# Kernel optimization log

Hardware: AMD Instinct MI355X
Metric: run time of the kernel (lower is better)

The kernel has to match this reference:

```python
import jax, jax.numpy as jnp
import numpy as np

NG, NT, E = 2500, 20000, 640000
SRC_DIM, DST_DIM, HID, OUT, NCLS = 128, 500, 128, 128, 16


def setup_inputs() -> dict:
    key = jax.random.key(0)
    ks = jax.random.split(key, 11)
    d = {
        "gene_feats": jax.random.normal(ks[0], (NG, SRC_DIM), jnp.float32),
        "train_feats": jax.random.normal(ks[1], (NT, DST_DIM), jnp.float32),
        "edge_src": jax.random.randint(ks[2], (E,), 0, NG),
        "edge_dst": jax.random.randint(ks[3], (E,), 0, NT),
        # conv1: SAGEConv((src_dim, dst_dim) -> hidden)
        "W1_neigh": jax.random.normal(ks[4], (SRC_DIM, HID), jnp.float32) / np.sqrt(SRC_DIM),
        "W1_self": jax.random.normal(ks[5], (DST_DIM, HID), jnp.float32) / np.sqrt(DST_DIM),
        "b1": jnp.zeros((HID,), jnp.float32),
        # conv2: SAGEConv(hidden -> out); src input is the raw gene features
        "W2_neigh": jax.random.normal(ks[6], (HID, OUT), jnp.float32) / np.sqrt(HID),
        "W2_self": jax.random.normal(ks[7], (HID, OUT), jnp.float32) / np.sqrt(HID),
        "b2": jnp.zeros((OUT,), jnp.float32),
        # classifier MLP
        "Wc1": jax.random.normal(ks[8], (OUT, OUT), jnp.float32) / np.sqrt(OUT),
        "bc1": jnp.zeros((OUT,), jnp.float32),
        "Wc2": jax.random.normal(ks[9], (OUT, NCLS), jnp.float32) / np.sqrt(OUT),
        "bc2": jnp.zeros((NCLS,), jnp.float32),
    }
    return d


def _segment_mean(msgs, dst, num_segments):
    # mean over in-edges; isolated dst nodes get 0 (DGL convention)
    sums = jax.ops.segment_sum(msgs, dst, num_segments=num_segments)
    cnt = jax.ops.segment_sum(jnp.ones((msgs.shape[0],), msgs.dtype), dst,
                              num_segments=num_segments)
    return sums / jnp.maximum(cnt, 1.0)[:, None]


def reference(gene_feats, train_feats, edge_src, edge_dst,
              W1_neigh, W1_self, b1, W2_neigh, W2_self, b2,
              Wc1, bc1, Wc2, bc2):
    # mean-aggregate gene (src) features onto train (dst) nodes
    agg = _segment_mean(gene_feats[edge_src], edge_dst, NT)  # [NT, SRC_DIM]
    # conv1: fc_self(h_dst) + fc_neigh(mean_neigh) + bias, then ReLU
    h1 = jax.nn.relu(train_feats @ W1_self + agg @ W1_neigh + b1)  # [NT, HID]
    # conv2 reuses raw gene features as src -> same mean aggregation
    h2 = jax.nn.relu(h1 @ W2_self + agg @ W2_neigh + b2)  # [NT, OUT]
    # classifier: Linear -> ReLU -> Linear
    return jax.nn.relu(h2 @ Wc1 + bc1) @ Wc2 + bc2  # [NT, NCLS]
```

## Files before the change

### kernel.cpp

```cpp
#include <hip/hip_runtime.h>


#define NG 2500
#define NT 20000
#define NE 640000
#define NCLS 16
#define CAP 96
#define NTILE 1250

typedef unsigned short u16;
typedef unsigned int u32;

typedef float f32x4 __attribute__((ext_vector_type(4)));
typedef __bf16 bf16x8 __attribute__((ext_vector_type(8)));

__device__ __forceinline__ float b2f(u16 u) { return __uint_as_float(((u32)u) << 16); }
__device__ __forceinline__ float blo(u32 p) { return __uint_as_float(p << 16); }
__device__ __forceinline__ float bhi(u32 p) { return __uint_as_float(p & 0xffff0000u); }
__device__ __forceinline__ u16 f2b(float f) {
    u32 u = __float_as_uint(f);
    return (u16)((u + 0x7fffu + ((u >> 16) & 1u)) >> 16);
}

#define B1N 81920
#define B2N 32768
#define B3N 16384
#define B4N 2048
#define NEB 2500
#define CVB NTILE
#define GNB 625
#define PKB 520

__global__ __launch_bounds__(256) void k_prep(
    const int* __restrict__ esrc, const int* __restrict__ edst,
    int* __restrict__ cnt, u16* __restrict__ csr,
    const float* __restrict__ train, const float* __restrict__ gene,
    u16* __restrict__ AF, u32* __restrict__ GH32,
    const float* __restrict__ W1n, const float* __restrict__ W1s,
    const float* __restrict__ W2n, const float* __restrict__ W2s,
    const float* __restrict__ Wc1, const float* __restrict__ Wc2,
    u16* __restrict__ B1h, u16* __restrict__ B1l,
    u16* __restrict__ B2h, u16* __restrict__ B2l,
    u16* __restrict__ B3h, u16* __restrict__ B3l,
    u16* __restrict__ B4h, u16* __restrict__ B4l) {
    int blk = blockIdx.x, t = threadIdx.x;
    if (blk < NEB) {
        int e = blk * 256 + t;
        if (e < NE) {
            unsigned d = (unsigned)edst[e];
            if (d < NT) {
                int slot = atomicAdd(&cnt[d], 1);
                if (slot < CAP) csr[(size_t)d * CAP + slot] = (u16)esrc[e];
            }
        }
        return;
    }
    if (blk < NEB + CVB) {
        __shared__ __align__(16) u16 L[16 * 520];
        u32* L32 = (u32*)L;
        int tile = blk - NEB;
        for (int i = t; i < 160; i += 256) {
            int r = i / 10, c = i - r * 10;
            L32[r * 260 + 250 + c] = 0;
        }
        for (int i = t; i < 2000; i += 256) {
            int r = i / 125, c4 = i - r * 125;
            float4 v = *(const float4*)(train + (size_t)(tile * 16 + r) * 500 + c4 * 4);
            int base = r * 260 + c4 * 2;
            L32[base] = (u32)f2b(v.x) | ((u32)f2b(v.y) << 16);
            L32[base + 1] = (u32)f2b(v.z) | ((u32)f2b(v.w) << 16);
        }
        __syncthreads();
#pragma unroll
        for (int it = 0; it < 4; ++it) {
            int slot = t + it * 256;
            int kk = slot >> 6, lane = slot & 63;
            int m = lane & 15, q = lane >> 4;
            uint4 v = *(const uint4*)(L + m * 520 + kk * 32 + q * 8);
            *(uint4*)(AF + (((size_t)tile * 16 + kk) * 64 + lane) * 8) = v;
        }
        return;
    }
    if (blk < NEB + CVB + GNB) {
        int idx = (blk - NEB - CVB) * 256 + t;
        float2 v = ((const float2*)gene)[idx];
        GH32[idx] = (u32)f2b(v.x) | ((u32)f2b(v.y) << 16);
        return;
    }
    int idx = (blk - NEB - CVB - GNB) * 256 + t;
    float v = 0.f;
    u16 *ph = 0, *pl = 0;
    int off = 0;
    if (idx < B1N) {
        int j = idx & 7, l = (idx >> 3) & 63, rest = idx >> 9;
        int g = rest & 7, kk = rest >> 3;
        int k = kk * 32 + ((l >> 4) << 3) + j, n = (g << 4) + (l & 15);
        if (k < 500) v = W1s[k * 128 + n];
        else if (k >= 512) v = W1n[(k - 512) * 128 + n];
        ph = B1h; pl = B1l; off = idx;
    } else if (idx < B1N + B2N) {
        int e = idx - B1N;
        int j = e & 7, l = (e >> 3) & 63, rest = e >> 9;
        int g = rest & 7, kk = rest >> 3;
        int k = kk * 32 + ((l >> 4) << 3) + j, n = (g << 4) + (l & 15);
        v = (k < 128) ? W2s[k * 128 + n] : W2n[(k - 128) * 128 + n];
        ph = B2h; pl = B2l; off = e;
    } else if (idx < B1N + B2N + B3N) {
        int e = idx - (B1N + B2N);
        int j = e & 7, l = (e >> 3) & 63, rest = e >> 9;
        int g = rest & 7, kk = rest >> 3;
        int k = kk * 32 + ((l >> 4) << 3) + j, n = (g << 4) + (l & 15);
        v = Wc1[k * 128 + n];
        ph = B3h; pl = B3l; off = e;
    } else if (idx < B1N + B2N + B3N + B4N) {
        int e = idx - (B1N + B2N + B3N);
        int j = e & 7, l = (e >> 3) & 63, kk = e >> 9;
        int k = kk * 32 + ((l >> 4) << 3) + j, n = l & 15;
        v = Wc2[k * 16 + n];
        ph = B4h; pl = B4l; off = e;
    }
    if (ph) {
        u16 hi = f2b(v);
        u16 lo = f2b(v - b2f(hi));
        ph[off] = hi;
        pl[off] = lo;
    }
}

__global__ __launch_bounds__(512) void k_mega(
    const int* __restrict__ cnt, const u16* __restrict__ csr,
    const u16* __restrict__ GH, const u16* __restrict__ AF,
    const u16* __restrict__ B1h, const u16* __restrict__ B1l,
    const u16* __restrict__ B2h, const u16* __restrict__ B2l,
    const u16* __restrict__ B3h, const u16* __restrict__ B3l,
    const u16* __restrict__ B4h, const u16* __restrict__ B4l,
    const float* __restrict__ b1, const float* __restrict__ b2,
    const float* __restrict__ bc1, const float* __restrict__ bc2,
    float* __restrict__ out) {
    __shared__ __align__(16) u16 SAGh[32 * 136], SAGl[32 * 136];
    __shared__ __align__(16) u16 S1h[32 * 136], S1l[32 * 136];
    __shared__ __align__(16) u16 S2h[32 * 136], S2l[32 * 136];
    int t = threadIdx.x;
    int row0 = blockIdx.x * 32;

    {
        int r = t >> 4, cg = t & 15;
        int d = row0 + r;
        int ctrue = cnt[d];
        int c = ctrue > CAP ? CAP : ctrue;
        const u16* crow = csr + (size_t)d * CAP;
        float a[8];
#pragma unroll
        for (int p = 0; p < 8; ++p) a[p] = 0.f;
        int j = 0;
        for (; j + 1 < c; j += 2) {
            int s0 = crow[j], s1 = crow[j + 1];
            uint4 p0 = *(const uint4*)(GH + (size_t)s0 * 128 + cg * 8);
            uint4 p1 = *(const uint4*)(GH + (size_t)s1 * 128 + cg * 8);
            a[0] += blo(p0.x); a[1] += bhi(p0.x);
            a[2] += blo(p0.y); a[3] += bhi(p0.y);
            a[4] += blo(p0.z); a[5] += bhi(p0.z);
            a[6] += blo(p0.w); a[7] += bhi(p0.w);
            a[0] += blo(p1.x); a[1] += bhi(p1.x);
            a[2] += blo(p1.y); a[3] += bhi(p1.y);
            a[4] += blo(p1.z); a[5] += bhi(p1.z);
            a[6] += blo(p1.w); a[7] += bhi(p1.w);
        }
        if (j < c) {
            int s = crow[j];
            uint4 p0 = *(const uint4*)(GH + (size_t)s * 128 + cg * 8);
            a[0] += blo(p0.x); a[1] += bhi(p0.x);
            a[2] += blo(p0.y); a[3] += bhi(p0.y);
            a[4] += blo(p0.z); a[5] += bhi(p0.z);
            a[6] += blo(p0.w); a[7] += bhi(p0.w);
        }
        float inv = (ctrue > 0) ? 1.f / (float)ctrue : 0.f;
        int base = (r * 136 + cg * 8) >> 1;
        u32* SH = (u32*)SAGh;
        u32* SL = (u32*)SAGl;
#pragma unroll
        for (int p = 0; p < 4; ++p) {
            float x = a[2 * p] * inv, y = a[2 * p + 1] * inv;
            u16 hx = f2b(x), hy = f2b(y);
            SH[base + p] = (u32)hx | ((u32)hy << 16);
            SL[base + p] = (u32)f2b(x - b2f(hx)) | ((u32)f2b(y - b2f(hy)) << 16);
        }
    }
    __syncthreads();

    int lane = t & 63, g = t >> 6;
    int m = lane & 15, q = lane >> 4, n16 = lane & 15;
    size_t tile0 = (size_t)blockIdx.x * 2;

    const u16* aB0 = AF + ((tile0 * 16) * 64 + lane) * 8;
    const u16* aB1 = AF + (((tile0 + 1) * 16) * 64 + lane) * 8;
    int hr0 = m * 136 + q * 8;
    int hr1 = (16 + m) * 136 + q * 8;
    int cr0 = q * 4, cr1 = 16 + q * 4;
    const f32x4 z4 = {0.f, 0.f, 0.f, 0.f};
    f32x4 acc0 = z4, acc1 = z4;

#pragma unroll 4
    for (int kk = 0; kk < 16; ++kk) {
        bf16x8 a0 = *(const bf16x8*)(aB0 + kk * 512);
        bf16x8 a1 = *(const bf16x8*)(aB1 + kk * 512);
        size_t bo = ((size_t)(kk * 8 + g) * 64 + lane) * 8;
        bf16x8 bh = *(const bf16x8*)(B1h + bo);
        bf16x8 bl = *(const bf16x8*)(B1l + bo);
        acc0 = __builtin_amdgcn_mfma_f32_16x16x32_bf16(a0, bh, acc0, 0, 0, 0);
        acc0 = __builtin_amdgcn_mfma_f32_16x16x32_bf16(a0, bl, acc0, 0, 0, 0);
        acc1 = __builtin_amdgcn_mfma_f32_16x16x32_bf16(a1, bh, acc1, 0, 0, 0);
        acc1 = __builtin_amdgcn_mfma_f32_16x16x32_bf16(a1, bl, acc1, 0, 0, 0);
    }
#pragma unroll
    for (int kk = 16; kk < 20; ++kk) {
        int o = (kk - 16) * 32;
        bf16x8 ah0 = *(const bf16x8*)(SAGh + hr0 + o);
        bf16x8 al0 = *(const bf16x8*)(SAGl + hr0 + o);
        bf16x8 ah1 = *(const bf16x8*)(SAGh + hr1 + o);
        bf16x8 al1 = *(const bf16x8*)(SAGl + hr1 + o);
        size_t bo = ((size_t)(kk * 8 + g) * 64 + lane) * 8;
        bf16x8 bh = *(const bf16x8*)(B1h + bo);
        bf16x8 bl = *(const bf16x8*)(B1l + bo);
        acc0 = __builtin_amdgcn_mfma_f32_16x16x32_bf16(ah0, bh, acc0, 0, 0, 0);
        acc0 = __builtin_amdgcn_mfma_f32_16x16x32_bf16(ah0, bl, acc0, 0, 0, 0);
        acc0 = __builtin_amdgcn_mfma_f32_16x16x32_bf16(al0, bh, acc0, 0, 0, 0);
        acc1 = __builtin_amdgcn_mfma_f32_16x16x32_bf16(ah1, bh, acc1, 0, 0, 0);
        acc1 = __builtin_amdgcn_mfma_f32_16x16x32_bf16(ah1, bl, acc1, 0, 0, 0);
        acc1 = __builtin_amdgcn_mfma_f32_16x16x32_bf16(al1, bh, acc1, 0, 0, 0);
    }
    {
        int n = g * 16 + n16;
        float bias = b1[n];
#pragma unroll
        for (int rg = 0; rg < 4; ++rg) {
            float v0 = acc0[rg] + bias; v0 = v0 > 0.f ? v0 : 0.f;
            float v1 = acc1[rg] + bias; v1 = v1 > 0.f ? v1 : 0.f;
            u16 h0 = f2b(v0), h1v = f2b(v1);
            S1h[(cr0 + rg) * 136 + n] = h0; S1l[(cr0 + rg) * 136 + n] = f2b(v0 - b2f(h0));
            S1h[(cr1 + rg) * 136 + n] = h1v; S1l[(cr1 + rg) * 136 + n] = f2b(v1 - b2f(h1v));
        }
    }
    __syncthreads();

    acc0 = z4; acc1 = z4;
#pragma unroll
    for (int kk = 0; kk < 8; ++kk) {
        const u16* Ph = (kk < 4) ? S1h : SAGh;
        const u16* Pl = (kk < 4) ? S1l : SAGl;
        int o = (kk & 3) * 32;
        bf16x8 ah0 = *(const bf16x8*)(Ph + hr0 + o);
        bf16x8 al0 = *(const bf16x8*)(Pl + hr0 + o);
        bf16x8 ah1 = *(const bf16x8*)(Ph + hr1 + o);
        bf16x8 al1 = *(const bf16x8*)(Pl + hr1 + o);
        size_t bo = ((size_t)(kk * 8 + g) * 64 + lane) * 8;
        bf16x8 bh = *(const bf16x8*)(B2h + bo);
        bf16x8 bl = *(const bf16x8*)(B2l + bo);
        acc0 = __builtin_amdgcn_mfma_f32_16x16x32_bf16(ah0, bh, acc0, 0, 0, 0);
        acc0 = __builtin_amdgcn_mfma_f32_16x16x32_bf16(ah0, bl, acc0, 0, 0, 0);
        acc0 = __builtin_amdgcn_mfma_f32_16x16x32_bf16(al0, bh, acc0, 0, 0, 0);
        acc1 = __builtin_amdgcn_mfma_f32_16x16x32_bf16(ah1, bh, acc1, 0, 0, 0);
        acc1 = __builtin_amdgcn_mfma_f32_16x16x32_bf16(ah1, bl, acc1, 0, 0, 0);
        acc1 = __builtin_amdgcn_mfma_f32_16x16x32_bf16(al1, bh, acc1, 0, 0, 0);
    }
    {
        int n = g * 16 + n16;
        float bias = b2[n];
#pragma unroll
        for (int rg = 0; rg < 4; ++rg) {
            float v0 = acc0[rg] + bias; v0 = v0 > 0.f ? v0 : 0.f;
            float v1 = acc1[rg] + bias; v1 = v1 > 0.f ? v1 : 0.f;
            u16 h0 = f2b(v0), h1v = f2b(v1);
            S2h[(cr0 + rg) * 136 + n] = h0; S2l[(cr0 + rg) * 136 + n] = f2b(v0 - b2f(h0));
            S2h[(cr1 + rg) * 136 + n] = h1v; S2l[(cr1 + rg) * 136 + n] = f2b(v1 - b2f(h1v));
        }
    }
    __syncthreads();

    acc0 = z4; acc1 = z4;
#pragma unroll
    for (int kk = 0; kk < 4; ++kk) {
        int o = kk * 32;
        bf16x8 ah0 = *(const bf16x8*)(S2h + hr0 + o);
        bf16x8 al0 = *(const bf16x8*)(S2l + hr0 + o);
        bf16x8 ah1 = *(const bf16x8*)(S2h + hr1 + o);
        bf16x8 al1 = *(const bf16x8*)(S2l + hr1 + o);
        size_t bo = ((size_t)(kk * 8 + g) * 64 + lane) * 8;
        bf16x8 bh = *(const bf16x8*)(B3h + bo);
        bf16x8 bl = *(const bf16x8*)(B3l + bo);
        acc0 = __builtin_amdgcn_mfma_f32_16x16x32_bf16(ah0, bh, acc0, 0, 0, 0);
        acc0 = __builtin_amdgcn_mfma_f32_16x16x32_bf16(ah0, bl, acc0, 0, 0, 0);
        acc0 = __builtin_amdgcn_mfma_f32_16x16x32_bf16(al0, bh, acc0, 0, 0, 0);
        acc1 = __builtin_amdgcn_mfma_f32_16x16x32_bf16(ah1, bh, acc1, 0, 0, 0);
        acc1 = __builtin_amdgcn_mfma_f32_16x16x32_bf16(ah1, bl, acc1, 0, 0, 0);
        acc1 = __builtin_amdgcn_mfma_f32_16x16x32_bf16(al1, bh, acc1, 0, 0, 0);
    }
    {
        int n = g * 16 + n16;
        float bias = bc1[n];
#pragma unroll
        for (int rg = 0; rg < 4; ++rg) {
            float v0 = acc0[rg] + bias; v0 = v0 > 0.f ? v0 : 0.f;
            float v1 = acc1[rg] + bias; v1 = v1 > 0.f ? v1 : 0.f;
            u16 h0 = f2b(v0), h1v = f2b(v1);
            S1h[(cr0 + rg) * 136 + n] = h0; S1l[(cr0 + rg) * 136 + n] = f2b(v0 - b2f(h0));
            S1h[(cr1 + rg) * 136 + n] = h1v; S1l[(cr1 + rg) * 136 + n] = f2b(v1 - b2f(h1v));
        }
    }
    __syncthreads();

    if (g < 2) {
        int hr = (g == 0) ? hr0 : hr1;
        int cr = (g == 0) ? cr0 : cr1;
        f32x4 a4 = z4;
#pragma unroll
        for (int kk = 0; kk < 4; ++kk) {
            bf16x8 ah = *(const bf16x8*)(S1h + hr + kk * 32);
            bf16x8 al = *(const bf16x8*)(S1l + hr + kk * 32);
            size_t bo = ((size_t)kk * 64 + lane) * 8;
            bf16x8 bh = *(const bf16x8*)(B4h + bo);
            bf16x8 bl = *(const bf16x8*)(B4l + bo);
            a4 = __builtin_amdgcn_mfma_f32_16x16x32_bf16(ah, bh, a4, 0, 0, 0);
            a4 = __builtin_amdgcn_mfma_f32_16x16x32_bf16(ah, bl, a4, 0, 0, 0);
            a4 = __builtin_amdgcn_mfma_f32_16x16x32_bf16(al, bh, a4, 0, 0, 0);
        }
        float bias = bc2[n16];
#pragma unroll
        for (int rg = 0; rg < 4; ++rg)
            out[(size_t)(row0 + cr + rg) * NCLS + n16] = a4[rg] + bias;
    }
}

extern "C" void kernel_launch(void* const* d_in, const int* in_sizes, int n_in,
                              void* d_out, int out_size, void* d_ws, size_t ws_size,
                              hipStream_t stream) {
    const float* gene = (const float*)d_in[0];
    const float* train = (const float*)d_in[1];
    const int* esrc = (const int*)d_in[2];
    const int* edst = (const int*)d_in[3];

    char* ws = (char*)d_ws;
    int* cnt = (int*)(ws + 0);
    u16* csr = (u16*)(ws + 80000);
    u16* AF = (u16*)(ws + 3920000);
    u16* GH = (u16*)(ws + 24400000);
    u16* B1h = (u16*)(ws + 25040000);
    u16* B1l = (u16*)(ws + 25203840);
    u16* B2h = (u16*)(ws + 25367680);
    u16* B2l = (u16*)(ws + 25433216);
    u16* B3h = (u16*)(ws + 25498752);
    u16* B3l = (u16*)(ws + 25531520);
    u16* B4h = (u16*)(ws + 25564288);
    u16* B4l = (u16*)(ws + 25568384);

    hipMemsetAsync(cnt, 0, NT * sizeof(int), stream);
    k_prep<<<NEB + CVB + GNB + PKB, 256, 0, stream>>>(
        esrc, edst, cnt, csr, train, gene, AF, (u32*)GH,
        (const float*)d_in[4], (const float*)d_in[5], (const float*)d_in[7],
        (const float*)d_in[8], (const float*)d_in[10], (const float*)d_in[12],
        B1h, B1l, B2h, B2l, B3h, B3l, B4h, B4l);
    k_mega<<<NT / 32, 512, 0, stream>>>(
        cnt, csr, GH, AF, B1h, B1l, B2h, B2l, B3h, B3l, B4h, B4l,
        (const float*)d_in[6], (const float*)d_in[9], (const float*)d_in[11],
        (const float*)d_in[13], (float*)d_out);
}
```

Before: 179.1 us.

## Partition edge bucketing per XCD to localize atomics and CSR writes

Edge bucketing now reads the XCC id from a hardware register, and each of the 8 XCDs gets its own count array and CSR slab (capacity 40 per destination per XCD). The intent is to keep atomic contention and scattered writes within one die's L2 instead of bouncing cache lines across dies. In exchange the aggregation loop in the main kernel must read eight counts and eight CSR rows per destination. The memset grows eightfold and the workspace grows. Per-XCD overflow past 40 entries would silently drop edges.

```diff
diff --git a/kernel.cpp b/kernel.cpp
--- a/kernel.cpp
+++ b/kernel.cpp
@@ -5,7 +5,7 @@
 #define NT 20000
 #define NE 640000
 #define NCLS 16
-#define CAP 96
+#define CAP8 40
 #define NTILE 1250
 
 typedef unsigned short u16;
@@ -33,7 +33,7 @@
 
 __global__ __launch_bounds__(256) void k_prep(
     const int* __restrict__ esrc, const int* __restrict__ edst,
-    int* __restrict__ cnt, u16* __restrict__ csr,
+    int* __restrict__ cnt8, u16* __restrict__ csr8,
     const float* __restrict__ train, const float* __restrict__ gene,
     u16* __restrict__ AF, u32* __restrict__ GH32,
     const float* __restrict__ W1n, const float* __restrict__ W1s,
@@ -45,12 +45,15 @@
     u16* __restrict__ B4h, u16* __restrict__ B4l) {
     int blk = blockIdx.x, t = threadIdx.x;
     if (blk < NEB) {
+        int xcc = __builtin_amdgcn_s_getreg(63508) & 7;
+        int* mycnt = cnt8 + (size_t)xcc * NT;
+        u16* mycsr = csr8 + (size_t)xcc * NT * CAP8;
         int e = blk * 256 + t;
         if (e < NE) {
             unsigned d = (unsigned)edst[e];
             if (d < NT) {
-                int slot = atomicAdd(&cnt[d], 1);
-                if (slot < CAP) csr[(size_t)d * CAP + slot] = (u16)esrc[e];
+                int slot = atomicAdd(&mycnt[d], 1);
+                if (slot < CAP8) mycsr[(size_t)d * CAP8 + slot] = (u16)esrc[e];
             }
         }
         return;
@@ -128,7 +131,7 @@
 }
 
 __global__ __launch_bounds__(512) void k_mega(
-    const int* __restrict__ cnt, const u16* __restrict__ csr,
+    const int* __restrict__ cnt8, const u16* __restrict__ csr8,
     const u16* __restrict__ GH, const u16* __restrict__ AF,
     const u16* __restrict__ B1h, const u16* __restrict__ B1l,
     const u16* __restrict__ B2h, const u16* __restrict__ B2l,
@@ -146,35 +149,40 @@
     {
         int r = t >> 4, cg = t & 15;
         int d = row0 + r;
-        int ctrue = cnt[d];
-        int c = ctrue > CAP ? CAP : ctrue;
-        const u16* crow = csr + (size_t)d * CAP;
         float a[8];
 #pragma unroll
         for (int p = 0; p < 8; ++p) a[p] = 0.f;
-        int j = 0;
-        for (; j + 1 < c; j += 2) {
-            int s0 = crow[j], s1 = crow[j + 1];
-            uint4 p0 = *(const uint4*)(GH + (size_t)s0 * 128 + cg * 8);
-            uint4 p1 = *(const uint4*)(GH + (size_t)s1 * 128 + cg * 8);
-            a[0] += blo(p0.x); a[1] += bhi(p0.x);
-            a[2] += blo(p0.y); a[3] += bhi(p0.y);
-            a[4] += blo(p0.z); a[5] += bhi(p0.z);
-            a[6] += blo(p0.w); a[7] += bhi(p0.w);
-            a[0] += blo(p1.x); a[1] += bhi(p1.x);
-            a[2] += blo(p1.y); a[3] += bhi(p1.y);
-            a[4] += blo(p1.z); a[5] += bhi(p1.z);
-            a[6] += blo(p1.w); a[7] += bhi(p1.w);
-        }
-        if (j < c) {
-            int s = crow[j];
-            uint4 p0 = *(const uint4*)(GH + (size_t)s * 128 + cg * 8);
-            a[0] += blo(p0.x); a[1] += bhi(p0.x);
-            a[2] += blo(p0.y); a[3] += bhi(p0.y);
-            a[4] += blo(p0.z); a[5] += bhi(p0.z);
-            a[6] += blo(p0.w); a[7] += bhi(p0.w);
-        }
-        float inv = (ctrue > 0) ? 1.f / (float)ctrue : 0.f;
+        int ctot = 0;
+#pragma unroll
+        for (int x = 0; x < 8; ++x) {
+            int craw = cnt8[(size_t)x * NT + d];
+            ctot += craw;
+            int c = craw > CAP8 ? CAP8 : craw;
+            const u16* crow = csr8 + ((size_t)x * NT + d) * CAP8;
+            int j = 0;
+            for (; j + 1 < c; j += 2) {
+                int s0 = crow[j], s1 = crow[j + 1];
+                uint4 p0 = *(const uint4*)(GH + (size_t)s0 * 128 + cg * 8);
+                uint4 p1 = *(const uint4*)(GH + (size_t)s1 * 128 + cg * 8);
+                a[0] += blo(p0.x); a[1] += bhi(p0.x);
+                a[2] += blo(p0.y); a[3] += bhi(p0.y);
+                a[4] += blo(p0.z); a[5] += bhi(p0.z);
+                a[6] += blo(p0.w); a[7] += bhi(p0.w);
+                a[0] += blo(p1.x); a[1] += bhi(p1.x);
+                a[2] += blo(p1.y); a[3] += bhi(p1.y);
+                a[4] += blo(p1.z); a[5] += bhi(p1.z);
+                a[6] += blo(p1.w); a[7] += bhi(p1.w);
+            }
+            if (j < c) {
+                int s = crow[j];
+                uint4 p0 = *(const uint4*)(GH + (size_t)s * 128 + cg * 8);
+                a[0] += blo(p0.x); a[1] += bhi(p0.x);
+                a[2] += blo(p0.y); a[3] += bhi(p0.y);
+                a[4] += blo(p0.z); a[5] += bhi(p0.z);
+                a[6] += blo(p0.w); a[7] += bhi(p0.w);
+            }
+        }
+        float inv = (ctot > 0) ? 1.f / (float)ctot : 0.f;
         int base = (r * 136 + cg * 8) >> 1;
         u32* SH = (u32*)SAGh;
         u32* SL = (u32*)SAGl;
@@ -340,27 +348,27 @@
     const int* edst = (const int*)d_in[3];
 
     char* ws = (char*)d_ws;
-    int* cnt = (int*)(ws + 0);
-    u16* csr = (u16*)(ws + 80000);
-    u16* AF = (u16*)(ws + 3920000);
-    u16* GH = (u16*)(ws + 24400000);
-    u16* B1h = (u16*)(ws + 25040000);
-    u16* B1l = (u16*)(ws + 25203840);
-    u16* B2h = (u16*)(ws + 25367680);
-    u16* B2l = (u16*)(ws + 25433216);
-    u16* B3h = (u16*)(ws + 25498752);
-    u16* B3l = (u16*)(ws + 25531520);
-    u16* B4h = (u16*)(ws + 25564288);
-    u16* B4l = (u16*)(ws + 25568384);
-
-    hipMemsetAsync(cnt, 0, NT * sizeof(int), stream);
+    int* cnt8 = (int*)(ws + 0);
+    u16* csr8 = (u16*)(ws + 640000);
+    u16* AF = (u16*)(ws + 13440000);
+    u16* GH = (u16*)(ws + 33920000);
+    u16* B1h = (u16*)(ws + 34560000);
+    u16* B1l = (u16*)(ws + 34723840);
+    u16* B2h = (u16*)(ws + 34887680);
+    u16* B2l = (u16*)(ws + 34953216);
+    u16* B3h = (u16*)(ws + 35018752);
+    u16* B3l = (u16*)(ws + 35051520);
+    u16* B4h = (u16*)(ws + 35084288);
+    u16* B4l = (u16*)(ws + 35088384);
+
+    hipMemsetAsync(cnt8, 0, 8 * NT * sizeof(int), stream);
     k_prep<<<NEB + CVB + GNB + PKB, 256, 0, stream>>>(
-        esrc, edst, cnt, csr, train, gene, AF, (u32*)GH,
+        esrc, edst, cnt8, csr8, train, gene, AF, (u32*)GH,
         (const float*)d_in[4], (const float*)d_in[5], (const float*)d_in[7],
         (const float*)d_in[8], (const float*)d_in[10], (const float*)d_in[12],
         B1h, B1l, B2h, B2l, B3h, B3l, B4h, B4l);
     k_mega<<<NT / 32, 512, 0, stream>>>(
-        cnt, csr, GH, AF, B1h, B1l, B2h, B2l, B3h, B3l, B4h, B4l,
+        cnt8, csr8, GH, AF, B1h, B1l, B2h, B2l, B3h, B3l, B4h, B4l,
         (const float*)d_in[6], (const float*)d_in[9], (const float*)d_in[11],
         (const float*)d_in[13], (float*)d_out);
 }
```

New measurement: 185.2 us. 1.03x slower.
